# Optimization experiments

Measured on AMD Instinct MI355X. Metric: run time of the kernel, lower is better.

## Reference

```python
import jax, jax.numpy as jnp
import numpy as np

NEG = -1e9


def _ln(x, g, b):
    m = x.mean(-1, keepdims=True)
    v = ((x - m) ** 2).mean(-1, keepdims=True)
    return (x - m) / jnp.sqrt(v + 1e-5) * g + b


def _block(single, pair, single_mask, pair_mask,
           pa_ln_g, pa_ln_b, pa_wqkv, pa_wg, pa_wout,
           pt_ln_g, pt_ln_b, pt_w1, pt_b1, pt_w2, pt_b2,
           sa_ln_g, sa_ln_b, sa_wq, sa_wkv, sa_wb, sa_wout,
           st_ln_g, st_ln_b, st_w1, st_b1, st_w2, st_b2):
    B, L, _, D = pair.shape
    H = sa_wb.shape[1]
    hd = D // H
    scale = 1.0 / jnp.sqrt(jnp.asarray(hd, dtype=pair.dtype))
    # ---- PairUpdate: PairAttention over L*L pseudo-tokens ----
    z = _ln(pair, pa_ln_g, pa_ln_b)                       # [B,L,L,D]
    N = L * L
    qkv = (z @ pa_wqkv).reshape(B, N, 3, H, hd)
    q = qkv[:, :, 0].transpose(0, 2, 1, 3)                # [B,H,N,hd]
    k = qkv[:, :, 1].transpose(0, 2, 1, 3)
    v = qkv[:, :, 2].transpose(0, 2, 1, 3)
    attn = jnp.einsum('bhid,bhjd->bhij', q, k) * scale    # [B,H,N,N]
    pm = pair_mask.reshape(B, 1, N)
    m = pm[:, :, :, None] * pm[:, :, None, :]             # [B,1,N,N]
    attn = jnp.where(m > 0, attn, NEG)
    attn = jax.nn.softmax(attn, axis=-1)
    out = jnp.einsum('bhij,bhjd->bhid', attn, v)          # [B,H,N,hd]
    out = out.transpose(0, 2, 1, 3).reshape(B, L, L, D)
    g = jax.nn.sigmoid(z @ pa_wg)
    out = (out @ pa_wout) * g * pair_mask[..., None]
    pair = pair + out
    t = _ln(pair, pt_ln_g, pt_ln_b)
    t = jax.nn.relu(t @ pt_w1 + pt_b1) @ pt_w2 + pt_b2
    pair = pair + t * pair_mask[..., None]
    # ---- SingleUpdate: AttentionPairBias ----
    s = _ln(single, sa_ln_g, sa_ln_b)                     # [B,L,D]
    q = (s @ sa_wq).reshape(B, L, H, hd)
    kv = (s @ sa_wkv).reshape(B, L, 2, H, hd)
    k2, v2 = kv[:, :, 0], kv[:, :, 1]
    attn = jnp.einsum('bihd,bjhd->bhij', q, k2) * scale   # [B,H,L,L]
    bias = (pair @ sa_wb).transpose(0, 3, 1, 2)           # [B,H,L,L]
    attn = attn + bias
    sm = single_mask[:, None, None, :]
    attn = jnp.where(sm > 0, attn, NEG)
    attn = jax.nn.softmax(attn, axis=-1)
    out = jnp.einsum('bhij,bjhd->bihd', attn, v2).reshape(B, L, D)
    single = single + (out @ sa_wout) * single_mask[..., None]
    # single transition
    t = _ln(single, st_ln_g, st_ln_b)
    t = jax.nn.relu(t @ st_w1 + st_b1) @ st_w2 + st_b2
    single = single + t * single_mask[..., None]
    return single, pair


def setup_inputs() -> dict:
    key = jax.random.key(0)
    B, L, D, H = 1, 64, 144, 8
    ks = iter(jax.random.split(key, 40))
    def nrm(shape, scale=0.02):
        return jax.random.normal(next(ks), shape, dtype=jnp.float32) * scale
    sm = jnp.ones((B, L), jnp.float32).at[:, L - 8:].set(0.0)
    pm = sm[:, :, None] * sm[:, None, :]
    return dict(
        single=jax.random.normal(next(ks), (B, L, D), jnp.float32),
        pair=jax.random.normal(next(ks), (B, L, L, D), jnp.float32),
        single_mask=sm,
        pair_mask=pm,
        pa_ln_g=jnp.ones((D,), jnp.float32), pa_ln_b=jnp.zeros((D,), jnp.float32),
        pa_wqkv=nrm((D, 3 * D)), pa_wg=nrm((D, D)), pa_wout=nrm((D, D)),
        pt_ln_g=jnp.ones((D,), jnp.float32), pt_ln_b=jnp.zeros((D,), jnp.float32),
        pt_w1=nrm((D, 4 * D)), pt_b1=jnp.zeros((4 * D,), jnp.float32),
        pt_w2=nrm((4 * D, D)), pt_b2=jnp.zeros((D,), jnp.float32),
        sa_ln_g=jnp.ones((D,), jnp.float32), sa_ln_b=jnp.zeros((D,), jnp.float32),
        sa_wq=nrm((D, D)), sa_wkv=nrm((D, 2 * D)), sa_wb=nrm((D, H)), sa_wout=nrm((D, D)),
        st_ln_g=jnp.ones((D,), jnp.float32), st_ln_b=jnp.zeros((D,), jnp.float32),
        st_w1=nrm((D, 4 * D)), st_b1=jnp.zeros((4 * D,), jnp.float32),
        st_w2=nrm((4 * D, D)), st_b2=jnp.zeros((D,), jnp.float32),
    )


def reference(single, pair, single_mask, pair_mask,
              pa_ln_g, pa_ln_b, pa_wqkv, pa_wg, pa_wout,
              pt_ln_g, pt_ln_b, pt_w1, pt_b1, pt_w2, pt_b2,
              sa_ln_g, sa_ln_b, sa_wq, sa_wkv, sa_wb, sa_wout,
              st_ln_g, st_ln_b, st_w1, st_b1, st_w2, st_b2):
    return _block(single, pair, single_mask, pair_mask,
                  pa_ln_g, pa_ln_b, pa_wqkv, pa_wg, pa_wout,
                  pt_ln_g, pt_ln_b, pt_w1, pt_b1, pt_w2, pt_b2,
                  sa_ln_g, sa_ln_b, sa_wq, sa_wkv, sa_wb, sa_wout,
                  st_ln_g, st_ln_b, st_w1, st_b1, st_w2, st_b2)
```

## Files before the change

kernel.cpp:

```cpp
#include <hip/hip_runtime.h>
#include <hip/hip_bf16.h>

typedef __hip_bfloat16 bf16;
typedef __attribute__((ext_vector_type(8))) short short8;
typedef __attribute__((ext_vector_type(16))) float floatx16;
typedef __attribute__((ext_vector_type(4))) unsigned int uint4v;

__device__ __forceinline__ float tof(bf16 x){ return __bfloat162float(x); }
__device__ __forceinline__ float bflo(unsigned u){ return __uint_as_float(u<<16); }
__device__ __forceinline__ float bfhi(unsigned u){ return __uint_as_float(u & 0xFFFF0000u); }
__device__ __forceinline__ float ldT(const void* p, long i, bool isf){
  return isf ? ((const float*)p)[i] : tof(((const bf16*)p)[i]);
}
__device__ __forceinline__ void stT(void* p, long i, bool isf, float v){
  if (isf) ((float*)p)[i] = v; else ((bf16*)p)[i] = __float2bfloat16(v);
}

#define LL 64
#define DD 144
#define NN 4096
#define HH 8
#define HDIM 18
#define SCALE 0.23570226039551584f
#define LOG2E 1.4426950408889634f

__global__ __launch_bounds__(256) void prep_weights(const unsigned* __restrict__ smaskw,
    int* __restrict__ dflag,
    const void* __restrict__ wqkv, const void* __restrict__ wg,
    const void* __restrict__ wout, const void* __restrict__ w1, const void* __restrict__ w2,
    const void* __restrict__ swq, const void* __restrict__ swkv,
    const void* __restrict__ swout, const void* __restrict__ sw1, const void* __restrict__ sw2,
    bf16* __restrict__ F1, bf16* __restrict__ Fout, bf16* __restrict__ Fw1,
    bf16* __restrict__ Fw2, bf16* __restrict__ Fs1, bf16* __restrict__ Wtswout,
    bf16* __restrict__ Wtst1, bf16* __restrict__ Wtst2){
  bool isf = (smaskw[0] == 0x3F800000u);
  if (blockIdx.x==0 && threadIdx.x==0) dflag[0] = isf ? 4 : 2;
  long t = (long)blockIdx.x*256 + threadIdx.x;
  if (t < 82944){
    int j=t&7, lane=(int)((t>>3)&63); long tk=t>>9; int ks=tk%9, tile=tk/9;
    int col=tile*32+(lane&31); int k=ks*16+(lane>>5)*8+j;
    float v = (col<432)? ldT(wqkv,(long)k*432+col,isf) : ldT(wg,(long)k*144+(col-432),isf);
    F1[t]=__float2bfloat16(v); return;
  } t -= 82944;
  if (t < 23040){
    int j=t&7, lane=(int)((t>>3)&63); long tk=t>>9; int ks=tk%9, tile=tk/9;
    int col=tile*32+(lane&31); if (col>143) col=143;
    int k=ks*16+(lane>>5)*8+j;
    Fout[t]=__float2bfloat16(ldT(wout,(long)k*144+col,isf)); return;
  } t -= 23040;
  if (t < 82944){
    int j=t&7, lane=(int)((t>>3)&63); long tk=t>>9; int ks=tk%9, tile=tk/9;
    int col=tile*32+(lane&31); int k=ks*16+(lane>>5)*8+j;
    Fw1[t]=__float2bfloat16(ldT(w1,(long)k*576+col,isf)); return;
  } t -= 82944;
  if (t < 92160){
    int j=t&7, lane=(int)((t>>3)&63); long tk=t>>9; int ks=tk%36, tile=tk/36;
    int col=tile*32+(lane&31); if (col>143) col=143;
    int k=ks*16+(lane>>5)*8+j;
    Fw2[t]=__float2bfloat16(ldT(w2,(long)k*144+col,isf)); return;
  } t -= 92160;
  if (t < 64512){
    int j=t&7, lane=(int)((t>>3)&63); long tk=t>>9; int ks=tk%9, tile=tk/9;
    int col=tile*32+(lane&31); if (col>431) col=431;
    int k=ks*16+(lane>>5)*8+j;
    float v = (col<144)? ldT(swq,(long)k*144+col,isf) : ldT(swkv,(long)k*288+(col-144),isf);
    Fs1[t]=__float2bfloat16(v); return;
  } t -= 64512;
  if (t < 20736){ int c=t/144,k=t-(long)c*144; Wtswout[t]=__float2bfloat16(ldT(swout,(long)k*144+c,isf)); return; }
  t -= 20736;
  if (t < 82944){ int c=t/144,k=t-(long)c*144; Wtst1[t]=__float2bfloat16(ldT(sw1,(long)k*576+c,isf)); return; }
  t -= 82944;
  if (t < 82944){ int c=t/576,k=t-(long)c*576; Wtst2[t]=__float2bfloat16(ldT(sw2,(long)k*144+c,isf)); return; }
}

__global__ __launch_bounds__(256) void gemm_fused1(const int* __restrict__ df,
    const void* __restrict__ pairv, const void* __restrict__ lng, const void* __restrict__ lnb,
    const bf16* __restrict__ F1,
    const void* __restrict__ pmask,
    bf16* __restrict__ Qb, bf16* __restrict__ Kf, bf16* __restrict__ Vf,
    bf16* __restrict__ gbuf,
    const void* __restrict__ singlev, const void* __restrict__ sag, const void* __restrict__ sab,
    const bf16* __restrict__ Fs1,
    bf16* __restrict__ q_sb, bf16* __restrict__ kv_sb){
  __shared__ short As[64*152];
  bool isf = df[0]==4;
  int tid=threadIdx.x, lane=tid&63, l31=lane&31, w=tid>>6, wr=w>>1, wc=w&1;
  int g=(lane>>5)*8;

  if (blockIdx.y == 64){
    if (blockIdx.x >= 7) return;
    for (int rr=w; rr<64; rr+=4){
      long base=(long)rr*DD;
      float e0=ldT(singlev,base+lane,isf), e1=ldT(singlev,base+lane+64,isf);
      float e2=(lane<16)?ldT(singlev,base+lane+128,isf):0.f;
      float s=e0+e1+e2;
      #pragma unroll
      for (int o=32;o;o>>=1) s += __shfl_xor(s,o);
      float mean=s*(1.f/144.f);
      float d0=e0-mean, d1=e1-mean, d2=(lane<16)?(e2-mean):0.f;
      float v=d0*d0+d1*d1+d2*d2;
      #pragma unroll
      for (int o=32;o;o>>=1) v += __shfl_xor(v,o);
      float rstd=rsqrtf(v*(1.f/144.f)+1e-5f);
      bf16 h0=__float2bfloat16(d0*rstd*ldT(sag,lane,isf)+ldT(sab,lane,isf));
      bf16 h1=__float2bfloat16(d1*rstd*ldT(sag,lane+64,isf)+ldT(sab,lane+64,isf));
      As[rr*152+lane]=*reinterpret_cast<short*>(&h0);
      As[rr*152+lane+64]=*reinterpret_cast<short*>(&h1);
      if (lane<16){
        bf16 h2=__float2bfloat16(d2*rstd*ldT(sag,lane+128,isf)+ldT(sab,lane+128,isf));
        As[rr*152+lane+128]=*reinterpret_cast<short*>(&h2);
      }
    }
    __syncthreads();
    int tile = blockIdx.x*2 + wc;
    const short8* wf = (const short8*)Fs1;
    floatx16 acc;
    #pragma unroll
    for (int i=0;i<16;i++) acc[i]=0.f;
    #pragma unroll
    for (int ks=0; ks<9; ks++){
      short8 af = *(const short8*)&As[(l31+32*wr)*152 + ks*16 + g];
      acc = __builtin_amdgcn_mfma_f32_32x32x16_bf16(af, wf[(tile*9+ks)*64+lane], acc, 0,0,0);
    }
    int col = tile*32 + l31;
    if (col < 432){
      #pragma unroll
      for (int r=0;r<16;r++){
        int row = 32*wr + (r&3)+8*(r>>2)+4*(lane>>5);
        if (col<144) q_sb[(size_t)row*DD+col] = __float2bfloat16(acc[r]);
        else kv_sb[(size_t)row*288+(col-144)] = __float2bfloat16(acc[r]);
      }
    }
    return;
  }

  int row0 = blockIdx.y*64, col0 = blockIdx.x*64;
  for (int rr=w; rr<64; rr+=4){
    long base=(long)(row0+rr)*DD;
    float e0=ldT(pairv,base+lane,isf), e1=ldT(pairv,base+lane+64,isf);
    float e2=(lane<16)?ldT(pairv,base+lane+128,isf):0.f;
    float s=e0+e1+e2;
    #pragma unroll
    for (int o=32;o;o>>=1) s += __shfl_xor(s,o);
    float mean=s*(1.f/144.f);
    float d0=e0-mean, d1=e1-mean, d2=(lane<16)?(e2-mean):0.f;
    float v=d0*d0+d1*d1+d2*d2;
    #pragma unroll
    for (int o=32;o;o>>=1) v += __shfl_xor(v,o);
    float rstd=rsqrtf(v*(1.f/144.f)+1e-5f);
    bf16 h0=__float2bfloat16(d0*rstd*ldT(lng,lane,isf)+ldT(lnb,lane,isf));
    bf16 h1=__float2bfloat16(d1*rstd*ldT(lng,lane+64,isf)+ldT(lnb,lane+64,isf));
    As[rr*152+lane]=*reinterpret_cast<short*>(&h0);
    As[rr*152+lane+64]=*reinterpret_cast<short*>(&h1);
    if (lane<16){
      bf16 h2=__float2bfloat16(d2*rstd*ldT(lng,lane+128,isf)+ldT(lnb,lane+128,isf));
      As[rr*152+lane+128]=*reinterpret_cast<short*>(&h2);
    }
  }
  __syncthreads();
  int tile = blockIdx.x*2 + wc;
  const short8* wf = (const short8*)F1;
  floatx16 acc;
  #pragma unroll
  for (int i=0;i<16;i++) acc[i]=0.f;
  #pragma unroll
  for (int ks=0; ks<9; ks++){
    short8 af = *(const short8*)&As[(l31+32*wr)*152 + ks*16 + g];
    acc = __builtin_amdgcn_mfma_f32_32x32x16_bf16(af, wf[(tile*9+ks)*64+lane], acc, 0,0,0);
  }
  int col = col0 + wc*32 + l31;
  #pragma unroll
  for (int r=0;r<16;r++){
    int row = row0 + 32*wr + (r&3)+8*(r>>2)+4*(lane>>5);
    if (col < 144){
      int hh = col/18, d = col - hh*18;
      Qb[((size_t)hh*NN+row)*32 + d] = __float2bfloat16(acc[r]*(SCALE*LOG2E));
    } else if (col < 288){
      int c2 = col-144, hh = c2/18, d = c2 - hh*18;
      int f = d>>4, rem = d&15, gs = rem>>3, j = rem&7;
      Kf[((((size_t)hh*128 + (row>>5))*2 + f)*64 + gs*32 + (row&31))*8 + j]
        = __float2bfloat16(acc[r]);
    } else if (col < 432){
      int c2 = col-288, hh = c2/18, d = c2 - hh*18;
      float pm = (ldT(pmask,row,isf)>0.f)?1.f:0.f;
      int kin = row&31, f = kin>>4, k15 = kin&15;
      int gs = (k15>>2)&1, j = (k15&3) | (((k15>>3)&1)<<2);
      Vf[((((size_t)hh*128 + (row>>5))*2 + f)*64 + gs*32 + d)*8 + j]
        = __float2bfloat16(acc[r]*pm);
    } else {
      int c2 = col-432;
      float gt = 1.f/(1.f+__expf(fminf(-acc[r],30.f)));
      gbuf[(size_t)row*DD+c2] = __float2bfloat16(gt);
    }
  }
  if (blockIdx.x==0){
    for (int t=threadIdx.x; t<64*8*7; t+=256){
      int n = row0 + t/56; int rem = t%56; int hh = rem/7, dw = rem%7 + 9;
      ((unsigned*)(Qb + ((size_t)hh*NN+n)*32))[dw] = 0;
    }
    for (int t=threadIdx.x; t<64*8; t+=256){
      int n = row0 + (t>>3), hh = t&7;
      float pm = (ldT(pmask,n,isf)>0.f)?1.f:0.f;
      int kin = n&31, f = kin>>4, k15 = kin&15;
      int gs = (k15>>2)&1, j = (k15&3) | (((k15>>3)&1)<<2);
      Vf[((((size_t)hh*128 + (n>>5))*2 + f)*64 + gs*32 + 18)*8 + j] = __float2bfloat16(pm);
    }
  }
}

__global__ __launch_bounds__(256) void pair_attn_mfma(const int* __restrict__ df,
    const bf16* __restrict__ Qb, const bf16* __restrict__ Kf,
    const bf16* __restrict__ Vf, bf16* __restrict__ aob){
  __shared__ float Comb[4][32][20];
  int h = blockIdx.x & 7, qt = blockIdx.x >> 3;
  int tid = threadIdx.x;
  int w = tid >> 6, lane = tid & 63;
  int l31 = lane & 31, gsel = lane>>5;

  const unsigned* qp = (const unsigned*)(Qb + ((size_t)h*NN + qt*32 + l31)*32);
  short8 qf0, qf1;
  #pragma unroll
  for (int j=0;j<4;j++) ((unsigned*)&qf0)[j] = qp[gsel*4+j];
  #pragma unroll
  for (int j=0;j<4;j++) ((unsigned*)&qf1)[j] = qp[8+gsel*4+j];

  floatx16 o;
  #pragma unroll
  for (int i=0;i<16;i++) o[i]=0.f;

  const short8* kf8 = (const short8*)Kf + (size_t)h*16384;
  const short8* vf8 = (const short8*)Vf + (size_t)h*16384;
  int c0 = w*32;

  short8 af0 = kf8[(c0*2+0)*64 + lane];
  short8 af1 = kf8[(c0*2+1)*64 + lane];
  short8 av0 = vf8[(c0*2+0)*64 + lane];
  short8 av1 = vf8[(c0*2+1)*64 + lane];

  for (int cc=0; cc<32; cc++){
    int cn = c0 + (cc<31 ? cc+1 : 31);
    short8 naf0 = kf8[(cn*2+0)*64 + lane];
    short8 naf1 = kf8[(cn*2+1)*64 + lane];
    short8 nav0 = vf8[(cn*2+0)*64 + lane];
    short8 nav1 = vf8[(cn*2+1)*64 + lane];

    floatx16 s;
    #pragma unroll
    for (int i=0;i<16;i++) s[i]=0.f;
    __builtin_amdgcn_s_setprio(1);
    s = __builtin_amdgcn_mfma_f32_32x32x16_bf16(af0, qf0, s, 0,0,0);
    s = __builtin_amdgcn_mfma_f32_32x32x16_bf16(af1, qf1, s, 0,0,0);
    __builtin_amdgcn_s_setprio(0);

    short8 P1, P2;
    #pragma unroll
    for (int j=0;j<4;j++){
      unsigned e0 = __float_as_uint(__builtin_amdgcn_exp2f(s[2*j]));
      unsigned e1 = __float_as_uint(__builtin_amdgcn_exp2f(s[2*j+1]));
      ((unsigned*)&P1)[j] = (e0>>16) | (e1 & 0xFFFF0000u);
      unsigned e2 = __float_as_uint(__builtin_amdgcn_exp2f(s[8+2*j]));
      unsigned e3 = __float_as_uint(__builtin_amdgcn_exp2f(s[9+2*j]));
      ((unsigned*)&P2)[j] = (e2>>16) | (e3 & 0xFFFF0000u);
    }

    __builtin_amdgcn_s_setprio(1);
    o = __builtin_amdgcn_mfma_f32_32x32x16_bf16(av0, P1, o, 0,0,0);
    o = __builtin_amdgcn_mfma_f32_32x32x16_bf16(av1, P2, o, 0,0,0);
    __builtin_amdgcn_s_setprio(0);

    af0=naf0; af1=naf1; av0=nav0; av1=nav1;
  }

  #pragma unroll
  for (int r=0;r<16;r++){
    int d = (r&3) + 8*(r>>2) + 4*gsel;
    if (d < 20) Comb[w][l31][d] = o[r];
  }
  __syncthreads();
  for (int t=tid; t<32*HDIM; t+=256){
    int q = t/HDIM, d = t-q*HDIM;
    float num = Comb[0][q][d]+Comb[1][q][d]+Comb[2][q][d]+Comb[3][q][d];
    float den = Comb[0][q][18]+Comb[1][q][18]+Comb[2][q][18]+Comb[3][q][18];
    aob[(size_t)(qt*32+q)*DD + h*HDIM + d] = __float2bfloat16(num/fmaxf(den,1e-20f));
  }
}

__global__ __launch_bounds__(512) void pair_tail(const int* __restrict__ df,
    const bf16* __restrict__ aob, const bf16* __restrict__ gbuf,
    const void* __restrict__ pairv, const void* __restrict__ pmaskv,
    const bf16* __restrict__ Fout, const void* __restrict__ ptln_g, const void* __restrict__ ptln_b,
    const bf16* __restrict__ Fw1, const void* __restrict__ b1v,
    const bf16* __restrict__ Fw2, const void* __restrict__ b2v,
    const void* __restrict__ wb, void* __restrict__ outP, long outOff,
    float* __restrict__ biasb){
  __shared__ __align__(16) char smem[65536];
  float* p1  = (float*)smem;
  short* ts  = (short*)(smem + 18432);
  short* hh_ = (short*)(smem + 28160);
  float* outv = (float*)(smem + 28160);

  bool isf = df[0]==4;
  int tid=threadIdx.x, lane=tid&63, l31=lane&31, gsel=lane>>5, g=gsel*8;
  int w=tid>>6;
  int r0 = blockIdx.x*32;
  const short8* foutf = (const short8*)Fout;
  const short8* fw1f  = (const short8*)Fw1;
  const short8* fw2f  = (const short8*)Fw2;

  for (int t=tid; t<32*72; t+=512){
    int m=t/72, dw=t%72;
    ((unsigned*)ts)[m*76+dw] = ((const unsigned*)(aob + (size_t)(r0+m)*144))[dw];
  }
  __syncthreads();

  for (int tile=w; tile<5; tile+=8){
    int c0=tile*32;
    floatx16 acc;
    #pragma unroll
    for (int i=0;i<16;i++) acc[i]=0.f;
    #pragma unroll
    for (int ks=0; ks<9; ks++){
      short8 af = *(const short8*)&ts[l31*152 + ks*16 + g];
      acc = __builtin_amdgcn_mfma_f32_32x32x16_bf16(af, foutf[(tile*9+ks)*64+lane], acc, 0,0,0);
    }
    if (c0+l31 < 144){
      #pragma unroll
      for (int r=0;r<16;r++){
        int row=(r&3)+8*(r>>2)+4*gsel;
        p1[row*144 + c0+l31] = acc[r];
      }
    }
  }
  __syncthreads();
  for (int t=tid; t<32*144; t+=512){
    int row=t/144; int col=t-row*144;
    long gidx=(long)(r0+row)*144 + col;
    float pm = (ldT(pmaskv, r0+row, isf)>0.f)?1.f:0.f;
    p1[t] = ldT(pairv,gidx,isf) + p1[t]*tof(gbuf[gidx])*pm;
  }
  __syncthreads();
  for (int rr=w; rr<32; rr+=8){
    float e0=p1[rr*144+lane], e1=p1[rr*144+lane+64], e2=(lane<16)?p1[rr*144+lane+128]:0.f;
    float s=e0+e1+e2;
    #pragma unroll
    for (int o=32;o;o>>=1) s += __shfl_xor(s,o);
    float mean=s*(1.f/144.f);
    float d0=e0-mean, d1=e1-mean, d2=(lane<16)?(e2-mean):0.f;
    float v=d0*d0+d1*d1+d2*d2;
    #pragma unroll
    for (int o=32;o;o>>=1) v += __shfl_xor(v,o);
    float rstd=rsqrtf(v*(1.f/144.f)+1e-5f);
    bf16 h0 = __float2bfloat16(d0*rstd*ldT(ptln_g,lane,isf)    + ldT(ptln_b,lane,isf));
    bf16 h1 = __float2bfloat16(d1*rstd*ldT(ptln_g,lane+64,isf) + ldT(ptln_b,lane+64,isf));
    ts[rr*152+lane]    = *reinterpret_cast<short*>(&h0);
    ts[rr*152+lane+64] = *reinterpret_cast<short*>(&h1);
    if (lane<16){
      bf16 h2 = __float2bfloat16(d2*rstd*ldT(ptln_g,lane+128,isf) + ldT(ptln_b,lane+128,isf));
      ts[rr*152+lane+128] = *reinterpret_cast<short*>(&h2);
    }
  }
  __syncthreads();
  for (int tile=w; tile<18; tile+=8){
    int c0=tile*32, colB=c0+l31;
    floatx16 acc;
    #pragma unroll
    for (int i=0;i<16;i++) acc[i]=0.f;
    #pragma unroll
    for (int ks=0; ks<9; ks++){
      short8 af = *(const short8*)&ts[l31*152 + ks*16 + g];
      acc = __builtin_amdgcn_mfma_f32_32x32x16_bf16(af, fw1f[(tile*9+ks)*64+lane], acc, 0,0,0);
    }
    float bb = ldT(b1v,colB,isf);
    #pragma unroll
    for (int r=0;r<16;r++){
      int row=(r&3)+8*(r>>2)+4*gsel;
      bf16 hv = __float2bfloat16(fmaxf(acc[r]+bb,0.f));
      hh_[row*584 + colB] = *reinterpret_cast<short*>(&hv);
    }
  }
  __syncthreads();
  floatx16 fin; int fc0 = -1;
  for (int tile=w; tile<5; tile+=8){
    int c0=tile*32;
    int colB=c0+l31; if (colB>143) colB=143;
    floatx16 acc;
    #pragma unroll
    for (int i=0;i<16;i++) acc[i]=0.f;
    #pragma unroll
    for (int ks=0; ks<36; ks++){
      short8 af = *(const short8*)&hh_[l31*584 + ks*16 + g];
      acc = __builtin_amdgcn_mfma_f32_32x32x16_bf16(af, fw2f[(tile*36+ks)*64+lane], acc, 0,0,0);
    }
    float bb = ldT(b2v,colB,isf);
    #pragma unroll
    for (int r=0;r<16;r++){
      int row=(r&3)+8*(r>>2)+4*gsel;
      float pm = (ldT(pmaskv, r0+row, isf)>0.f)?1.f:0.f;
      float val = p1[row*144 + colB] + (acc[r]+bb)*pm;
      if (c0+l31 < 144)
        stT(outP, outOff + (long)(r0+row)*144 + c0+l31, isf, val);
      fin[r]=val;
    }
    fc0 = c0;
  }
  __syncthreads();
  if (fc0 >= 0 && fc0+l31 < 144){
    #pragma unroll
    for (int r=0;r<16;r++){
      int row=(r&3)+8*(r>>2)+4*gsel;
      outv[row*144 + fc0+l31] = fin[r];
    }
  }
  __syncthreads();
  if (tid < 256){
    int n = tid>>3, hb = tid&7;
    float acc=0.f;
    #pragma unroll 4
    for (int k=0;k<144;k++) acc += outv[n*144+k]*ldT(wb,k*8+hb,isf);
    biasb[(size_t)(r0+n)*8+hb]=acc;
  }
}

__global__ __launch_bounds__(256) void single_tail(const int* __restrict__ df,
    const void* __restrict__ single, const bf16* __restrict__ q_sb,
    const bf16* __restrict__ kv_sb, const float* __restrict__ biasb,
    const void* __restrict__ smask, const bf16* __restrict__ Wtswout,
    const void* __restrict__ stln_g, const void* __restrict__ stln_b,
    const bf16* __restrict__ Wtst1, const void* __restrict__ st_b1,
    const bf16* __restrict__ Wtst2, const void* __restrict__ st_b2,
    void* __restrict__ outS){
  bool isf = df[0]==4;
  __shared__ __align__(16) short kvs[64*288];
  __shared__ float pexp[8][64];
  __shared__ float tot[8];
  __shared__ __align__(16) float bb[512];
  __shared__ float qs[DD], as_[DD], s1[DD], tss[DD], hs[576];
  __shared__ float mr[2];
  int n = blockIdx.x, tid = threadIdx.x;
  {
    const uint4v* src = (const uint4v*)kv_sb;
    uint4v* dst = (uint4v*)kvs;
    for (int t=tid; t<2304; t+=256) dst[t] = src[t];
  }
  if (tid<DD) qs[tid] = tof(q_sb[(size_t)n*DD+tid]);
  {
    const uint4v* src = (const uint4v*)(biasb + (size_t)n*512);
    uint4v* dst = (uint4v*)bb;
    if (tid<128) dst[tid] = src[tid];
  }
  __syncthreads();
  #pragma unroll
  for (int pp=0; pp<2; pp++){
    int pi = tid + pp*256;
    int h = pi>>6, j = pi&63;
    const unsigned* kr = (const unsigned*)&kvs[j*288 + h*HDIM];
    float s=0.f;
    #pragma unroll
    for (int i=0;i<9;i++){
      unsigned u = kr[i];
      s += qs[h*HDIM+2*i]*bflo(u) + qs[h*HDIM+2*i+1]*bfhi(u);
    }
    s = fminf(s*SCALE + bb[j*8+h], 30.f);
    pexp[h][j] = (ldT(smask,j,isf)>0.f) ? __expf(s) : 0.f;
  }
  __syncthreads();
  if (tid<64){
    int h=tid>>3, j0=(tid&7)*8;
    float t2=0.f;
    #pragma unroll
    for (int j=0;j<8;j++) t2 += pexp[h][j0+j];
    #pragma unroll
    for (int o=4;o;o>>=1) t2 += __shfl_xor(t2,o);
    if ((tid&7)==0) tot[h] = fmaxf(t2,1e-20f);
  }
  __syncthreads();
  if (tid<DD){
    int h = tid/HDIM;
    float a0=0.f, a1=0.f;
    #pragma unroll 8
    for (int j=0;j<64;j+=2){
      unsigned u0 = ((unsigned)(unsigned short)kvs[j*288 + 144 + tid])<<16;
      unsigned u1 = ((unsigned)(unsigned short)kvs[(j+1)*288 + 144 + tid])<<16;
      a0 += pexp[h][j]*__uint_as_float(u0);
      a1 += pexp[h][j+1]*__uint_as_float(u1);
    }
    as_[tid] = (a0+a1)/tot[h];
  }
  __syncthreads();
  float sm = ldT(smask,n,isf);
  if (tid<DD){
    const uint4v* wr = (const uint4v*)(Wtswout + (size_t)tid*DD);
    float a0=0.f, a1=0.f;
    #pragma unroll 3
    for (int kw=0; kw<18; kw+=2){
      uint4v u = wr[kw], u2 = wr[kw+1];
      a0 += as_[8*kw+0]*bflo(u[0]) + as_[8*kw+1]*bfhi(u[0])
          + as_[8*kw+2]*bflo(u[1]) + as_[8*kw+3]*bfhi(u[1])
          + as_[8*kw+4]*bflo(u[2]) + as_[8*kw+5]*bfhi(u[2])
          + as_[8*kw+6]*bflo(u[3]) + as_[8*kw+7]*bfhi(u[3]);
      a1 += as_[8*kw+8]*bflo(u2[0]) + as_[8*kw+9]*bfhi(u2[0])
          + as_[8*kw+10]*bflo(u2[1]) + as_[8*kw+11]*bfhi(u2[1])
          + as_[8*kw+12]*bflo(u2[2]) + as_[8*kw+13]*bfhi(u2[2])
          + as_[8*kw+14]*bflo(u2[3]) + as_[8*kw+15]*bfhi(u2[3]);
    }
    s1[tid] = ldT(single,(long)n*DD+tid,isf) + (a0+a1)*sm;
  }
  __syncthreads();
  if (tid < 64){
    float e0 = s1[tid], e1 = s1[tid+64], e2 = (tid<16)?s1[tid+128]:0.f;
    float s = e0+e1+e2;
    #pragma unroll
    for (int o=32;o;o>>=1) s += __shfl_xor(s,o);
    float mean = s*(1.f/144.f);
    float d0=e0-mean, d1=e1-mean, d2=(tid<16)?(e2-mean):0.f;
    float v = d0*d0+d1*d1+d2*d2;
    #pragma unroll
    for (int o=32;o;o>>=1) v += __shfl_xor(v,o);
    if (tid==0){ mr[0]=mean; mr[1]=rsqrtf(v*(1.f/144.f)+1e-5f); }
  }
  __syncthreads();
  if (tid<DD) tss[tid] = (s1[tid]-mr[0])*mr[1]*ldT(stln_g,tid,isf) + ldT(stln_b,tid,isf);
  __syncthreads();
  for (int c=tid;c<576;c+=256){
    const uint4v* wr = (const uint4v*)(Wtst1 + (size_t)c*DD);
    float a0=ldT(st_b1,c,isf), a1=0.f;
    #pragma unroll 3
    for (int kw=0; kw<18; kw+=2){
      uint4v u = wr[kw], u2 = wr[kw+1];
      a0 += tss[8*kw+0]*bflo(u[0]) + tss[8*kw+1]*bfhi(u[0])
          + tss[8*kw+2]*bflo(u[1]) + tss[8*kw+3]*bfhi(u[1])
          + tss[8*kw+4]*bflo(u[2]) + tss[8*kw+5]*bfhi(u[2])
          + tss[8*kw+6]*bflo(u[3]) + tss[8*kw+7]*bfhi(u[3]);
      a1 += tss[8*kw+8]*bflo(u2[0]) + tss[8*kw+9]*bfhi(u2[0])
          + tss[8*kw+10]*bflo(u2[1]) + tss[8*kw+11]*bfhi(u2[1])
          + tss[8*kw+12]*bflo(u2[2]) + tss[8*kw+13]*bfhi(u2[2])
          + tss[8*kw+14]*bflo(u2[3]) + tss[8*kw+15]*bfhi(u2[3]);
    }
    hs[c]=fmaxf(a0+a1,0.f);
  }
  __syncthreads();
  if (tid<DD){
    const uint4v* wr = (const uint4v*)(Wtst2 + (size_t)tid*576);
    float a0=ldT(st_b2,tid,isf), a1=0.f;
    #pragma unroll 4
    for (int kw=0; kw<72; kw+=2){
      uint4v u = wr[kw], u2 = wr[kw+1];
      a0 += hs[8*kw+0]*bflo(u[0]) + hs[8*kw+1]*bfhi(u[0])
          + hs[8*kw+2]*bflo(u[1]) + hs[8*kw+3]*bfhi(u[1])
          + hs[8*kw+4]*bflo(u[2]) + hs[8*kw+5]*bfhi(u[2])
          + hs[8*kw+6]*bflo(u[3]) + hs[8*kw+7]*bfhi(u[3]);
      a1 += hs[8*kw+8]*bflo(u2[0]) + hs[8*kw+9]*bfhi(u2[0])
          + hs[8*kw+10]*bflo(u2[1]) + hs[8*kw+11]*bfhi(u2[1])
          + hs[8*kw+12]*bflo(u2[2]) + hs[8*kw+13]*bfhi(u2[2])
          + hs[8*kw+14]*bflo(u2[3]) + hs[8*kw+15]*bfhi(u2[3]);
    }
    stT(outS,(long)n*DD+tid,isf, s1[tid] + (a0+a1)*sm);
  }
}

extern "C" void kernel_launch(void* const* d_in, const int* in_sizes, int n_in,
                              void* d_out, int out_size, void* d_ws, size_t ws_size,
                              hipStream_t stream) {
  char* wsb = (char*)d_ws;
  int*   dflag = (int*)wsb;
  bf16*  F1     = (bf16*)(wsb + 16);
  bf16*  Fout   = F1 + 82944;
  bf16*  Fw1    = Fout + 23040;
  bf16*  Fw2    = Fw1 + 82944;
  bf16*  Fs1    = Fw2 + 92160;
  bf16*  Wtswout= Fs1 + 64512;
  bf16*  Wtst1  = Wtswout + 20736;
  bf16*  Wtst2  = Wtst1 + 82944;
  bf16*  Qb   = Wtst2 + 82944;
  bf16*  Kf   = Qb + (size_t)HH*NN*32;
  bf16*  Vf   = Kf + (size_t)HH*131072;
  bf16*  gbuf = Vf + (size_t)HH*131072;
  bf16*  aob  = gbuf + (size_t)NN*DD;
  float* biasb= (float*)(aob + (size_t)NN*DD);
  bf16*  q_sb = (bf16*)(biasb + NN*8);
  bf16*  kv_sb= q_sb + LL*DD;

  const long OUTP_OFF = (long)LL*DD;

  prep_weights<<<2079,256,0,stream>>>((const unsigned*)d_in[2], dflag,
      d_in[6], d_in[7], d_in[8], d_in[11], d_in[13],
      d_in[17], d_in[18], d_in[20], d_in[23], d_in[25],
      F1, Fout, Fw1, Fw2, Fs1, Wtswout, Wtst1, Wtst2);

  gemm_fused1<<<dim3(9,65),256,0,stream>>>(dflag, d_in[1], d_in[4], d_in[5], F1, d_in[3],
                                           Qb, Kf, Vf, gbuf,
                                           d_in[0], d_in[15], d_in[16], Fs1, q_sb, kv_sb);
  pair_attn_mfma<<<1024,256,0,stream>>>(dflag, Qb, Kf, Vf, aob);
  pair_tail<<<128,512,0,stream>>>(dflag, aob, gbuf, d_in[1], d_in[3],
                                  Fout, d_in[9], d_in[10], Fw1, d_in[12],
                                  Fw2, d_in[14], d_in[19], d_out, OUTP_OFF, biasb);
  single_tail<<<LL,256,0,stream>>>(dflag, d_in[0], q_sb, kv_sb, biasb, d_in[2],
                                   Wtswout, d_in[21], d_in[22], Wtst1, d_in[24],
                                   Wtst2, d_in[26], d_out);
  (void)in_sizes; (void)n_in; (void)out_size; (void)ws_size;
}
```

Before: 225.2 us.

## Merge pair and single tails into one kernel with atomic-counter handoff

Fuses the pair_tail and single_tail kernels into a single 192-block launch of 1024-thread blocks. The first 128 blocks do the pair transition and publish bias rows, then bump a global counter. The other 64 blocks compute q·k scores, prefetch their weights into cache, and spin on the counter before applying the bias. This removes one launch and lets single-tail work overlap the pair tail. It also spreads the single-tail matvecs over more threads. It risks deadlock if the spinning blocks are not co-resident with the producers, and the pair-tail blocks now run 1024-thread blocks, which may hurt occupancy.

```diff
diff --git a/kernel.cpp b/kernel.cpp
--- a/kernel.cpp
+++ b/kernel.cpp
@@ -81,11 +81,13 @@
     bf16* __restrict__ gbuf,
     const void* __restrict__ singlev, const void* __restrict__ sag, const void* __restrict__ sab,
     const bf16* __restrict__ Fs1,
-    bf16* __restrict__ q_sb, bf16* __restrict__ kv_sb){
+    bf16* __restrict__ q_sb, bf16* __restrict__ kv_sb,
+    int* __restrict__ ctr){
   __shared__ short As[64*152];
   bool isf = df[0]==4;
   int tid=threadIdx.x, lane=tid&63, l31=lane&31, w=tid>>6, wr=w>>1, wc=w&1;
   int g=(lane>>5)*8;
+  if (blockIdx.x==0 && blockIdx.y==0 && tid==0) ctr[0]=0;
 
   if (blockIdx.y == 64){
     if (blockIdx.x >= 7) return;
@@ -285,276 +287,319 @@
   }
 }
 
-__global__ __launch_bounds__(512) void pair_tail(const int* __restrict__ df,
+__global__ __launch_bounds__(1024) void tails(const int* __restrict__ df,
     const bf16* __restrict__ aob, const bf16* __restrict__ gbuf,
     const void* __restrict__ pairv, const void* __restrict__ pmaskv,
     const bf16* __restrict__ Fout, const void* __restrict__ ptln_g, const void* __restrict__ ptln_b,
     const bf16* __restrict__ Fw1, const void* __restrict__ b1v,
     const bf16* __restrict__ Fw2, const void* __restrict__ b2v,
     const void* __restrict__ wb, void* __restrict__ outP, long outOff,
-    float* __restrict__ biasb){
-  __shared__ __align__(16) char smem[65536];
-  float* p1  = (float*)smem;
-  short* ts  = (short*)(smem + 18432);
-  short* hh_ = (short*)(smem + 28160);
-  float* outv = (float*)(smem + 28160);
-
-  bool isf = df[0]==4;
-  int tid=threadIdx.x, lane=tid&63, l31=lane&31, gsel=lane>>5, g=gsel*8;
-  int w=tid>>6;
-  int r0 = blockIdx.x*32;
-  const short8* foutf = (const short8*)Fout;
-  const short8* fw1f  = (const short8*)Fw1;
-  const short8* fw2f  = (const short8*)Fw2;
-
-  for (int t=tid; t<32*72; t+=512){
-    int m=t/72, dw=t%72;
-    ((unsigned*)ts)[m*76+dw] = ((const unsigned*)(aob + (size_t)(r0+m)*144))[dw];
-  }
-  __syncthreads();
-
-  for (int tile=w; tile<5; tile+=8){
-    int c0=tile*32;
-    floatx16 acc;
-    #pragma unroll
-    for (int i=0;i<16;i++) acc[i]=0.f;
-    #pragma unroll
-    for (int ks=0; ks<9; ks++){
-      short8 af = *(const short8*)&ts[l31*152 + ks*16 + g];
-      acc = __builtin_amdgcn_mfma_f32_32x32x16_bf16(af, foutf[(tile*9+ks)*64+lane], acc, 0,0,0);
-    }
-    if (c0+l31 < 144){
-      #pragma unroll
-      for (int r=0;r<16;r++){
-        int row=(r&3)+8*(r>>2)+4*gsel;
-        p1[row*144 + c0+l31] = acc[r];
-      }
-    }
-  }
-  __syncthreads();
-  for (int t=tid; t<32*144; t+=512){
-    int row=t/144; int col=t-row*144;
-    long gidx=(long)(r0+row)*144 + col;
-    float pm = (ldT(pmaskv, r0+row, isf)>0.f)?1.f:0.f;
-    p1[t] = ldT(pairv,gidx,isf) + p1[t]*tof(gbuf[gidx])*pm;
-  }
-  __syncthreads();
-  for (int rr=w; rr<32; rr+=8){
-    float e0=p1[rr*144+lane], e1=p1[rr*144+lane+64], e2=(lane<16)?p1[rr*144+lane+128]:0.f;
-    float s=e0+e1+e2;
-    #pragma unroll
-    for (int o=32;o;o>>=1) s += __shfl_xor(s,o);
-    float mean=s*(1.f/144.f);
-    float d0=e0-mean, d1=e1-mean, d2=(lane<16)?(e2-mean):0.f;
-    float v=d0*d0+d1*d1+d2*d2;
-    #pragma unroll
-    for (int o=32;o;o>>=1) v += __shfl_xor(v,o);
-    float rstd=rsqrtf(v*(1.f/144.f)+1e-5f);
-    bf16 h0 = __float2bfloat16(d0*rstd*ldT(ptln_g,lane,isf)    + ldT(ptln_b,lane,isf));
-    bf16 h1 = __float2bfloat16(d1*rstd*ldT(ptln_g,lane+64,isf) + ldT(ptln_b,lane+64,isf));
-    ts[rr*152+lane]    = *reinterpret_cast<short*>(&h0);
-    ts[rr*152+lane+64] = *reinterpret_cast<short*>(&h1);
-    if (lane<16){
-      bf16 h2 = __float2bfloat16(d2*rstd*ldT(ptln_g,lane+128,isf) + ldT(ptln_b,lane+128,isf));
-      ts[rr*152+lane+128] = *reinterpret_cast<short*>(&h2);
-    }
-  }
-  __syncthreads();
-  for (int tile=w; tile<18; tile+=8){
-    int c0=tile*32, colB=c0+l31;
-    floatx16 acc;
-    #pragma unroll
-    for (int i=0;i<16;i++) acc[i]=0.f;
-    #pragma unroll
-    for (int ks=0; ks<9; ks++){
-      short8 af = *(const short8*)&ts[l31*152 + ks*16 + g];
-      acc = __builtin_amdgcn_mfma_f32_32x32x16_bf16(af, fw1f[(tile*9+ks)*64+lane], acc, 0,0,0);
-    }
-    float bb = ldT(b1v,colB,isf);
-    #pragma unroll
-    for (int r=0;r<16;r++){
-      int row=(r&3)+8*(r>>2)+4*gsel;
-      bf16 hv = __float2bfloat16(fmaxf(acc[r]+bb,0.f));
-      hh_[row*584 + colB] = *reinterpret_cast<short*>(&hv);
-    }
-  }
-  __syncthreads();
-  floatx16 fin; int fc0 = -1;
-  for (int tile=w; tile<5; tile+=8){
-    int c0=tile*32;
-    int colB=c0+l31; if (colB>143) colB=143;
-    floatx16 acc;
-    #pragma unroll
-    for (int i=0;i<16;i++) acc[i]=0.f;
-    #pragma unroll
-    for (int ks=0; ks<36; ks++){
-      short8 af = *(const short8*)&hh_[l31*584 + ks*16 + g];
-      acc = __builtin_amdgcn_mfma_f32_32x32x16_bf16(af, fw2f[(tile*36+ks)*64+lane], acc, 0,0,0);
-    }
-    float bb = ldT(b2v,colB,isf);
-    #pragma unroll
-    for (int r=0;r<16;r++){
-      int row=(r&3)+8*(r>>2)+4*gsel;
-      float pm = (ldT(pmaskv, r0+row, isf)>0.f)?1.f:0.f;
-      float val = p1[row*144 + colB] + (acc[r]+bb)*pm;
-      if (c0+l31 < 144)
-        stT(outP, outOff + (long)(r0+row)*144 + c0+l31, isf, val);
-      fin[r]=val;
-    }
-    fc0 = c0;
-  }
-  __syncthreads();
-  if (fc0 >= 0 && fc0+l31 < 144){
-    #pragma unroll
-    for (int r=0;r<16;r++){
-      int row=(r&3)+8*(r>>2)+4*gsel;
-      outv[row*144 + fc0+l31] = fin[r];
-    }
-  }
-  __syncthreads();
-  if (tid < 256){
-    int n = tid>>3, hb = tid&7;
-    float acc=0.f;
-    #pragma unroll 4
-    for (int k=0;k<144;k++) acc += outv[n*144+k]*ldT(wb,k*8+hb,isf);
-    biasb[(size_t)(r0+n)*8+hb]=acc;
-  }
-}
-
-__global__ __launch_bounds__(256) void single_tail(const int* __restrict__ df,
-    const void* __restrict__ single, const bf16* __restrict__ q_sb,
-    const bf16* __restrict__ kv_sb, const float* __restrict__ biasb,
-    const void* __restrict__ smask, const bf16* __restrict__ Wtswout,
+    float* __restrict__ biasb,
+    const void* __restrict__ singlev, const bf16* __restrict__ q_sb,
+    const bf16* __restrict__ kv_sb, const void* __restrict__ smask,
+    const bf16* __restrict__ Wtswout,
     const void* __restrict__ stln_g, const void* __restrict__ stln_b,
     const bf16* __restrict__ Wtst1, const void* __restrict__ st_b1,
     const bf16* __restrict__ Wtst2, const void* __restrict__ st_b2,
-    void* __restrict__ outS){
+    void* __restrict__ outS, int* __restrict__ ctr){
+  __shared__ __align__(16) char smem[65536];
   bool isf = df[0]==4;
-  __shared__ __align__(16) short kvs[64*288];
-  __shared__ float pexp[8][64];
-  __shared__ float tot[8];
-  __shared__ __align__(16) float bb[512];
-  __shared__ float qs[DD], as_[DD], s1[DD], tss[DD], hs[576];
-  __shared__ float mr[2];
-  int n = blockIdx.x, tid = threadIdx.x;
-  {
-    const uint4v* src = (const uint4v*)kv_sb;
-    uint4v* dst = (uint4v*)kvs;
-    for (int t=tid; t<2304; t+=256) dst[t] = src[t];
-  }
-  if (tid<DD) qs[tid] = tof(q_sb[(size_t)n*DD+tid]);
-  {
-    const uint4v* src = (const uint4v*)(biasb + (size_t)n*512);
-    uint4v* dst = (uint4v*)bb;
-    if (tid<128) dst[tid] = src[tid];
-  }
-  __syncthreads();
-  #pragma unroll
-  for (int pp=0; pp<2; pp++){
-    int pi = tid + pp*256;
-    int h = pi>>6, j = pi&63;
-    const unsigned* kr = (const unsigned*)&kvs[j*288 + h*HDIM];
-    float s=0.f;
-    #pragma unroll
-    for (int i=0;i<9;i++){
-      unsigned u = kr[i];
-      s += qs[h*HDIM+2*i]*bflo(u) + qs[h*HDIM+2*i+1]*bfhi(u);
-    }
-    s = fminf(s*SCALE + bb[j*8+h], 30.f);
-    pexp[h][j] = (ldT(smask,j,isf)>0.f) ? __expf(s) : 0.f;
-  }
-  __syncthreads();
-  if (tid<64){
-    int h=tid>>3, j0=(tid&7)*8;
-    float t2=0.f;
-    #pragma unroll
-    for (int j=0;j<8;j++) t2 += pexp[h][j0+j];
-    #pragma unroll
-    for (int o=4;o;o>>=1) t2 += __shfl_xor(t2,o);
-    if ((tid&7)==0) tot[h] = fmaxf(t2,1e-20f);
-  }
-  __syncthreads();
-  if (tid<DD){
-    int h = tid/HDIM;
-    float a0=0.f, a1=0.f;
-    #pragma unroll 8
-    for (int j=0;j<64;j+=2){
-      unsigned u0 = ((unsigned)(unsigned short)kvs[j*288 + 144 + tid])<<16;
-      unsigned u1 = ((unsigned)(unsigned short)kvs[(j+1)*288 + 144 + tid])<<16;
-      a0 += pexp[h][j]*__uint_as_float(u0);
-      a1 += pexp[h][j+1]*__uint_as_float(u1);
-    }
-    as_[tid] = (a0+a1)/tot[h];
-  }
-  __syncthreads();
-  float sm = ldT(smask,n,isf);
-  if (tid<DD){
-    const uint4v* wr = (const uint4v*)(Wtswout + (size_t)tid*DD);
-    float a0=0.f, a1=0.f;
-    #pragma unroll 3
-    for (int kw=0; kw<18; kw+=2){
-      uint4v u = wr[kw], u2 = wr[kw+1];
-      a0 += as_[8*kw+0]*bflo(u[0]) + as_[8*kw+1]*bfhi(u[0])
-          + as_[8*kw+2]*bflo(u[1]) + as_[8*kw+3]*bfhi(u[1])
-          + as_[8*kw+4]*bflo(u[2]) + as_[8*kw+5]*bfhi(u[2])
-          + as_[8*kw+6]*bflo(u[3]) + as_[8*kw+7]*bfhi(u[3]);
-      a1 += as_[8*kw+8]*bflo(u2[0]) + as_[8*kw+9]*bfhi(u2[0])
-          + as_[8*kw+10]*bflo(u2[1]) + as_[8*kw+11]*bfhi(u2[1])
-          + as_[8*kw+12]*bflo(u2[2]) + as_[8*kw+13]*bfhi(u2[2])
-          + as_[8*kw+14]*bflo(u2[3]) + as_[8*kw+15]*bfhi(u2[3]);
-    }
-    s1[tid] = ldT(single,(long)n*DD+tid,isf) + (a0+a1)*sm;
-  }
-  __syncthreads();
-  if (tid < 64){
-    float e0 = s1[tid], e1 = s1[tid+64], e2 = (tid<16)?s1[tid+128]:0.f;
-    float s = e0+e1+e2;
-    #pragma unroll
-    for (int o=32;o;o>>=1) s += __shfl_xor(s,o);
-    float mean = s*(1.f/144.f);
-    float d0=e0-mean, d1=e1-mean, d2=(tid<16)?(e2-mean):0.f;
-    float v = d0*d0+d1*d1+d2*d2;
-    #pragma unroll
-    for (int o=32;o;o>>=1) v += __shfl_xor(v,o);
-    if (tid==0){ mr[0]=mean; mr[1]=rsqrtf(v*(1.f/144.f)+1e-5f); }
-  }
-  __syncthreads();
-  if (tid<DD) tss[tid] = (s1[tid]-mr[0])*mr[1]*ldT(stln_g,tid,isf) + ldT(stln_b,tid,isf);
-  __syncthreads();
-  for (int c=tid;c<576;c+=256){
-    const uint4v* wr = (const uint4v*)(Wtst1 + (size_t)c*DD);
-    float a0=ldT(st_b1,c,isf), a1=0.f;
-    #pragma unroll 3
-    for (int kw=0; kw<18; kw+=2){
-      uint4v u = wr[kw], u2 = wr[kw+1];
-      a0 += tss[8*kw+0]*bflo(u[0]) + tss[8*kw+1]*bfhi(u[0])
-          + tss[8*kw+2]*bflo(u[1]) + tss[8*kw+3]*bfhi(u[1])
-          + tss[8*kw+4]*bflo(u[2]) + tss[8*kw+5]*bfhi(u[2])
-          + tss[8*kw+6]*bflo(u[3]) + tss[8*kw+7]*bfhi(u[3]);
-      a1 += tss[8*kw+8]*bflo(u2[0]) + tss[8*kw+9]*bfhi(u2[0])
-          + tss[8*kw+10]*bflo(u2[1]) + tss[8*kw+11]*bfhi(u2[1])
-          + tss[8*kw+12]*bflo(u2[2]) + tss[8*kw+13]*bfhi(u2[2])
-          + tss[8*kw+14]*bflo(u2[3]) + tss[8*kw+15]*bfhi(u2[3]);
-    }
-    hs[c]=fmaxf(a0+a1,0.f);
-  }
-  __syncthreads();
-  if (tid<DD){
-    const uint4v* wr = (const uint4v*)(Wtst2 + (size_t)tid*576);
-    float a0=ldT(st_b2,tid,isf), a1=0.f;
-    #pragma unroll 4
-    for (int kw=0; kw<72; kw+=2){
-      uint4v u = wr[kw], u2 = wr[kw+1];
-      a0 += hs[8*kw+0]*bflo(u[0]) + hs[8*kw+1]*bfhi(u[0])
-          + hs[8*kw+2]*bflo(u[1]) + hs[8*kw+3]*bfhi(u[1])
-          + hs[8*kw+4]*bflo(u[2]) + hs[8*kw+5]*bfhi(u[2])
-          + hs[8*kw+6]*bflo(u[3]) + hs[8*kw+7]*bfhi(u[3]);
-      a1 += hs[8*kw+8]*bflo(u2[0]) + hs[8*kw+9]*bfhi(u2[0])
-          + hs[8*kw+10]*bflo(u2[1]) + hs[8*kw+11]*bfhi(u2[1])
-          + hs[8*kw+12]*bflo(u2[2]) + hs[8*kw+13]*bfhi(u2[2])
-          + hs[8*kw+14]*bflo(u2[3]) + hs[8*kw+15]*bfhi(u2[3]);
-    }
-    stT(outS,(long)n*DD+tid,isf, s1[tid] + (a0+a1)*sm);
+  int tid=threadIdx.x;
+  int bid = blockIdx.x;
+
+  if (bid < 128){
+    float* p1  = (float*)smem;
+    short* ts  = (short*)(smem + 18432);
+    short* hh_ = (short*)(smem + 28160);
+    float* outv = (float*)(smem + 28160);
+    int lane=tid&63, l31=lane&31, gsel=lane>>5, g=gsel*8;
+    int w=tid>>6;
+    int r0 = bid*32;
+    const short8* foutf = (const short8*)Fout;
+    const short8* fw1f  = (const short8*)Fw1;
+    const short8* fw2f  = (const short8*)Fw2;
+
+    for (int t=tid; t<32*72; t+=1024){
+      int m=t/72, dw=t%72;
+      ((unsigned*)ts)[m*76+dw] = ((const unsigned*)(aob + (size_t)(r0+m)*144))[dw];
+    }
+    __syncthreads();
+
+    for (int tile=w; tile<5; tile+=16){
+      int c0=tile*32;
+      floatx16 acc;
+      #pragma unroll
+      for (int i=0;i<16;i++) acc[i]=0.f;
+      #pragma unroll
+      for (int ks=0; ks<9; ks++){
+        short8 af = *(const short8*)&ts[l31*152 + ks*16 + g];
+        acc = __builtin_amdgcn_mfma_f32_32x32x16_bf16(af, foutf[(tile*9+ks)*64+lane], acc, 0,0,0);
+      }
+      if (c0+l31 < 144){
+        #pragma unroll
+        for (int r=0;r<16;r++){
+          int row=(r&3)+8*(r>>2)+4*gsel;
+          p1[row*144 + c0+l31] = acc[r];
+        }
+      }
+    }
+    __syncthreads();
+    for (int t=tid; t<32*144; t+=1024){
+      int row=t/144; int col=t-row*144;
+      long gidx=(long)(r0+row)*144 + col;
+      float pm = (ldT(pmaskv, r0+row, isf)>0.f)?1.f:0.f;
+      p1[t] = ldT(pairv,gidx,isf) + p1[t]*tof(gbuf[gidx])*pm;
+    }
+    __syncthreads();
+    for (int rr=w; rr<32; rr+=16){
+      float e0=p1[rr*144+lane], e1=p1[rr*144+lane+64], e2=(lane<16)?p1[rr*144+lane+128]:0.f;
+      float s=e0+e1+e2;
+      #pragma unroll
+      for (int o=32;o;o>>=1) s += __shfl_xor(s,o);
+      float mean=s*(1.f/144.f);
+      float d0=e0-mean, d1=e1-mean, d2=(lane<16)?(e2-mean):0.f;
+      float v=d0*d0+d1*d1+d2*d2;
+      #pragma unroll
+      for (int o=32;o;o>>=1) v += __shfl_xor(v,o);
+      float rstd=rsqrtf(v*(1.f/144.f)+1e-5f);
+      bf16 h0 = __float2bfloat16(d0*rstd*ldT(ptln_g,lane,isf)    + ldT(ptln_b,lane,isf));
+      bf16 h1 = __float2bfloat16(d1*rstd*ldT(ptln_g,lane+64,isf) + ldT(ptln_b,lane+64,isf));
+      ts[rr*152+lane]    = *reinterpret_cast<short*>(&h0);
+      ts[rr*152+lane+64] = *reinterpret_cast<short*>(&h1);
+      if (lane<16){
+        bf16 h2 = __float2bfloat16(d2*rstd*ldT(ptln_g,lane+128,isf) + ldT(ptln_b,lane+128,isf));
+        ts[rr*152+lane+128] = *reinterpret_cast<short*>(&h2);
+      }
+    }
+    __syncthreads();
+    for (int tile=w; tile<18; tile+=16){
+      int c0=tile*32, colB=c0+l31;
+      floatx16 acc;
+      #pragma unroll
+      for (int i=0;i<16;i++) acc[i]=0.f;
+      #pragma unroll
+      for (int ks=0; ks<9; ks++){
+        short8 af = *(const short8*)&ts[l31*152 + ks*16 + g];
+        acc = __builtin_amdgcn_mfma_f32_32x32x16_bf16(af, fw1f[(tile*9+ks)*64+lane], acc, 0,0,0);
+      }
+      float bbv = ldT(b1v,colB,isf);
+      #pragma unroll
+      for (int r=0;r<16;r++){
+        int row=(r&3)+8*(r>>2)+4*gsel;
+        bf16 hv = __float2bfloat16(fmaxf(acc[r]+bbv,0.f));
+        hh_[row*584 + colB] = *reinterpret_cast<short*>(&hv);
+      }
+    }
+    __syncthreads();
+    floatx16 fin; int fc0 = -1;
+    for (int tile=w; tile<5; tile+=16){
+      int c0=tile*32;
+      int colB=c0+l31; if (colB>143) colB=143;
+      floatx16 acc;
+      #pragma unroll
+      for (int i=0;i<16;i++) acc[i]=0.f;
+      #pragma unroll
+      for (int ks=0; ks<36; ks++){
+        short8 af = *(const short8*)&hh_[l31*584 + ks*16 + g];
+        acc = __builtin_amdgcn_mfma_f32_32x32x16_bf16(af, fw2f[(tile*36+ks)*64+lane], acc, 0,0,0);
+      }
+      float bbv = ldT(b2v,colB,isf);
+      #pragma unroll
+      for (int r=0;r<16;r++){
+        int row=(r&3)+8*(r>>2)+4*gsel;
+        float pm = (ldT(pmaskv, r0+row, isf)>0.f)?1.f:0.f;
+        float val = p1[row*144 + colB] + (acc[r]+bbv)*pm;
+        if (c0+l31 < 144)
+          stT(outP, outOff + (long)(r0+row)*144 + c0+l31, isf, val);
+        fin[r]=val;
+      }
+      fc0 = c0;
+    }
+    __syncthreads();
+    if (fc0 >= 0 && fc0+l31 < 144){
+      #pragma unroll
+      for (int r=0;r<16;r++){
+        int row=(r&3)+8*(r>>2)+4*gsel;
+        outv[row*144 + fc0+l31] = fin[r];
+      }
+    }
+    __syncthreads();
+    if (tid < 256){
+      int n = tid>>3, hb = tid&7;
+      float acc=0.f;
+      #pragma unroll 4
+      for (int k=0;k<144;k++) acc += outv[n*144+k]*ldT(wb,k*8+hb,isf);
+      biasb[(size_t)(r0+n)*8+hb]=acc;
+    }
+    __threadfence();
+    __syncthreads();
+    if (tid==0) atomicAdd(ctr,1);
+  } else {
+    int n = bid - 128;
+    short* kvs  = (short*)smem;
+    float* pexpv= (float*)(smem+36864);
+    float* bbv  = (float*)(smem+38912);
+    float* sraw = (float*)(smem+40960);
+    float* part = (float*)(smem+43008);
+    float* qs   = (float*)(smem+45312);
+    float* as_  = (float*)(smem+45888);
+    float* s1v  = (float*)(smem+46464);
+    float* tss  = (float*)(smem+47040);
+    float* hsv  = (float*)(smem+47616);
+    float* totv = (float*)(smem+49920);
+    float* mr   = (float*)(smem+49952);
+
+    {
+      const uint4v* src = (const uint4v*)kv_sb;
+      uint4v* dst = (uint4v*)kvs;
+      for (int t=tid; t<2304; t+=1024) dst[t] = src[t];
+    }
+    if (tid<DD) qs[tid] = tof(q_sb[(size_t)n*DD+tid]);
+    __syncthreads();
+    if (tid < 512){
+      int h = tid>>6, j = tid&63;
+      const unsigned* kr = (const unsigned*)&kvs[j*288 + h*HDIM];
+      float s=0.f;
+      #pragma unroll
+      for (int i=0;i<9;i++){
+        unsigned u = kr[i];
+        s += qs[h*HDIM+2*i]*bflo(u) + qs[h*HDIM+2*i+1]*bfhi(u);
+      }
+      sraw[tid] = s*SCALE;
+    }
+    {
+      float dm=0.f;
+      const uint4v* pw1=(const uint4v*)Wtst1;
+      for (int t=tid; t<10368; t+=1024){ uint4v u=pw1[t]; dm += bflo(u[0]); }
+      const uint4v* pw2=(const uint4v*)Wtst2;
+      for (int t=tid; t<10368; t+=1024){ uint4v u=pw2[t]; dm += bflo(u[0]); }
+      const uint4v* pw3=(const uint4v*)Wtswout;
+      for (int t=tid; t<2592; t+=1024){ uint4v u=pw3[t]; dm += bflo(u[0]); }
+      asm volatile("" :: "v"(dm));
+    }
+    if (tid==0){
+      while (__hip_atomic_load(ctr, __ATOMIC_ACQUIRE, __HIP_MEMORY_SCOPE_AGENT) < 128)
+        __builtin_amdgcn_s_sleep(8);
+    }
+    __syncthreads();
+    __threadfence();
+    {
+      const uint4v* src = (const uint4v*)(biasb + (size_t)n*512);
+      uint4v* dst = (uint4v*)bbv;
+      if (tid<128) dst[tid] = src[tid];
+    }
+    __syncthreads();
+    if (tid<512){
+      int h = tid>>6, j = tid&63;
+      float s = fminf(sraw[tid] + bbv[j*8+h], 30.f);
+      pexpv[tid] = (ldT(smask,j,isf)>0.f) ? __expf(s) : 0.f;
+    }
+    __syncthreads();
+    if (tid<64){
+      int h=tid>>3, j0=(tid&7)*8;
+      float t2=0.f;
+      #pragma unroll
+      for (int j=0;j<8;j++) t2 += pexpv[h*64+j0+j];
+      #pragma unroll
+      for (int o=4;o;o>>=1) t2 += __shfl_xor(t2,o);
+      if ((tid&7)==0) totv[h] = fmaxf(t2,1e-20f);
+    }
+    __syncthreads();
+    if (tid<576){
+      int seg=tid/144, d=tid-seg*144, h=d/HDIM, j0=seg*16;
+      float a0=0.f, a1=0.f;
+      #pragma unroll
+      for (int j=0;j<16;j+=2){
+        unsigned u0 = ((unsigned)(unsigned short)kvs[(j0+j)*288 + 144 + d])<<16;
+        unsigned u1 = ((unsigned)(unsigned short)kvs[(j0+j+1)*288 + 144 + d])<<16;
+        a0 += pexpv[h*64+j0+j]*__uint_as_float(u0);
+        a1 += pexpv[h*64+j0+j+1]*__uint_as_float(u1);
+      }
+      part[seg*144+d]=a0+a1;
+    }
+    __syncthreads();
+    if (tid<DD){
+      int h = tid/HDIM;
+      as_[tid] = (part[tid]+part[144+tid]+part[288+tid]+part[432+tid])/totv[h];
+    }
+    __syncthreads();
+    float smv = ldT(smask,n,isf);
+    if (tid<288){
+      int seg=tid/144, d=tid-seg*144;
+      const uint4v* wr = (const uint4v*)(Wtswout + (size_t)d*DD) + seg*9;
+      int b0=seg*72;
+      float a=0.f;
+      #pragma unroll
+      for (int kw=0; kw<9; kw++){
+        uint4v u = wr[kw]; int e=b0+8*kw;
+        a += as_[e]*bflo(u[0]) + as_[e+1]*bfhi(u[0])
+           + as_[e+2]*bflo(u[1]) + as_[e+3]*bfhi(u[1])
+           + as_[e+4]*bflo(u[2]) + as_[e+5]*bfhi(u[2])
+           + as_[e+6]*bflo(u[3]) + as_[e+7]*bfhi(u[3]);
+      }
+      part[seg*144+d]=a;
+    }
+    __syncthreads();
+    if (tid<DD) s1v[tid] = ldT(singlev,(long)n*DD+tid,isf) + (part[tid]+part[144+tid])*smv;
+    __syncthreads();
+    if (tid < 64){
+      float e0 = s1v[tid], e1 = s1v[tid+64], e2 = (tid<16)?s1v[tid+128]:0.f;
+      float s = e0+e1+e2;
+      #pragma unroll
+      for (int o=32;o;o>>=1) s += __shfl_xor(s,o);
+      float mean = s*(1.f/144.f);
+      float d0=e0-mean, d1=e1-mean, d2=(tid<16)?(e2-mean):0.f;
+      float v = d0*d0+d1*d1+d2*d2;
+      #pragma unroll
+      for (int o=32;o;o>>=1) v += __shfl_xor(v,o);
+      if (tid==0){ mr[0]=mean; mr[1]=rsqrtf(v*(1.f/144.f)+1e-5f); }
+    }
+    __syncthreads();
+    if (tid<DD) tss[tid] = (s1v[tid]-mr[0])*mr[1]*ldT(stln_g,tid,isf) + ldT(stln_b,tid,isf);
+    __syncthreads();
+    if (tid<576){
+      int c=tid;
+      const uint4v* wr = (const uint4v*)(Wtst1 + (size_t)c*DD);
+      float a0=ldT(st_b1,c,isf), a1=0.f;
+      #pragma unroll 3
+      for (int kw=0; kw<18; kw+=2){
+        uint4v u = wr[kw], u2 = wr[kw+1];
+        a0 += tss[8*kw+0]*bflo(u[0]) + tss[8*kw+1]*bfhi(u[0])
+            + tss[8*kw+2]*bflo(u[1]) + tss[8*kw+3]*bfhi(u[1])
+            + tss[8*kw+4]*bflo(u[2]) + tss[8*kw+5]*bfhi(u[2])
+            + tss[8*kw+6]*bflo(u[3]) + tss[8*kw+7]*bfhi(u[3]);
+        a1 += tss[8*kw+8]*bflo(u2[0]) + tss[8*kw+9]*bfhi(u2[0])
+            + tss[8*kw+10]*bflo(u2[1]) + tss[8*kw+11]*bfhi(u2[1])
+            + tss[8*kw+12]*bflo(u2[2]) + tss[8*kw+13]*bfhi(u2[2])
+            + tss[8*kw+14]*bflo(u2[3]) + tss[8*kw+15]*bfhi(u2[3]);
+      }
+      hsv[c]=fmaxf(a0+a1,0.f);
+    }
+    __syncthreads();
+    if (tid<576){
+      int seg=tid/144, d=tid-seg*144;
+      const uint4v* wr = (const uint4v*)(Wtst2 + (size_t)d*576) + seg*18;
+      int b0=seg*144;
+      float a0=0.f, a1=0.f;
+      #pragma unroll 3
+      for (int kw=0; kw<18; kw+=2){
+        uint4v u = wr[kw], u2 = wr[kw+1];
+        int e=b0+8*kw;
+        a0 += hsv[e]*bflo(u[0]) + hsv[e+1]*bfhi(u[0])
+            + hsv[e+2]*bflo(u[1]) + hsv[e+3]*bfhi(u[1])
+            + hsv[e+4]*bflo(u[2]) + hsv[e+5]*bfhi(u[2])
+            + hsv[e+6]*bflo(u[3]) + hsv[e+7]*bfhi(u[3]);
+        a1 += hsv[e+8]*bflo(u2[0]) + hsv[e+9]*bfhi(u2[0])
+            + hsv[e+10]*bflo(u2[1]) + hsv[e+11]*bfhi(u2[1])
+            + hsv[e+12]*bflo(u2[2]) + hsv[e+13]*bfhi(u2[2])
+            + hsv[e+14]*bflo(u2[3]) + hsv[e+15]*bfhi(u2[3]);
+      }
+      part[seg*144+d]=a0+a1;
+    }
+    __syncthreads();
+    if (tid<DD)
+      stT(outS,(long)n*DD+tid,isf,
+          s1v[tid] + (ldT(st_b2,tid,isf)+part[tid]+part[144+tid]+part[288+tid]+part[432+tid])*smv);
   }
 }
 
@@ -563,6 +608,7 @@
                               hipStream_t stream) {
   char* wsb = (char*)d_ws;
   int*   dflag = (int*)wsb;
+  int*   ctr   = (int*)(wsb + 4);
   bf16*  F1     = (bf16*)(wsb + 16);
   bf16*  Fout   = F1 + 82944;
   bf16*  Fw1    = Fout + 23040;
@@ -589,13 +635,13 @@
 
   gemm_fused1<<<dim3(9,65),256,0,stream>>>(dflag, d_in[1], d_in[4], d_in[5], F1, d_in[3],
                                            Qb, Kf, Vf, gbuf,
-                                           d_in[0], d_in[15], d_in[16], Fs1, q_sb, kv_sb);
+                                           d_in[0], d_in[15], d_in[16], Fs1, q_sb, kv_sb, ctr);
   pair_attn_mfma<<<1024,256,0,stream>>>(dflag, Qb, Kf, Vf, aob);
-  pair_tail<<<128,512,0,stream>>>(dflag, aob, gbuf, d_in[1], d_in[3],
-                                  Fout, d_in[9], d_in[10], Fw1, d_in[12],
-                                  Fw2, d_in[14], d_in[19], d_out, OUTP_OFF, biasb);
-  single_tail<<<LL,256,0,stream>>>(dflag, d_in[0], q_sb, kv_sb, biasb, d_in[2],
-                                   Wtswout, d_in[21], d_in[22], Wtst1, d_in[24],
-                                   Wtst2, d_in[26], d_out);
+  tails<<<192,1024,0,stream>>>(dflag, aob, gbuf, d_in[1], d_in[3],
+                               Fout, d_in[9], d_in[10], Fw1, d_in[12],
+                               Fw2, d_in[14], d_in[19], d_out, OUTP_OFF, biasb,
+                               d_in[0], q_sb, kv_sb, d_in[2],
+                               Wtswout, d_in[21], d_in[22], Wtst1, d_in[24],
+                               Wtst2, d_in[26], d_out, ctr);
   (void)in_sizes; (void)n_in; (void)out_size; (void)ws_size;
 }
```

After: 283.6 us. +25.9%, slower.
